# Optimization experiments

Hardware: AMD Instinct MI355X
Metric: run time of the kernel (lower is better)

Reference implementation:

```python
import jax, jax.numpy as jnp
import numpy as np

# Llama-3.2-1B-style int4-quantized decoder (4 layers, reduced vocab)
L, D, H, HD, KVH, DFF, V, B, S = 4, 2048, 32, 64, 8, 8192, 32000, 4, 1024
ROPE_THETA = 500000.0


def setup_inputs() -> dict:
    key = jax.random.key(0)
    ks = jax.random.split(key, 18)
    def qw(k, shape):  # int4 weights stored in int32 carrier, range [-8, 8)
        return jax.random.randint(k, shape, -8, 8, dtype=jnp.int32)
    def sc(k, shape):  # per-output-channel dequant scales
        return jax.random.uniform(k, shape, jnp.float32, 0.005, 0.02)
    DKV = KVH * HD
    return {
        "token_ids": jax.random.randint(ks[0], (B, S), 0, V, dtype=jnp.int32),
        "embed": jax.random.normal(ks[1], (V, D), jnp.float32) * 0.02,
        "gamma_attn": jnp.ones((L, D), jnp.float32),
        "gamma_mlp": jnp.ones((L, D), jnp.float32),
        "gamma_final": jnp.ones((D,), jnp.float32),
        "wq": qw(ks[2], (L, D, D)),   "sq": sc(ks[3], (L, D)),
        "wk": qw(ks[4], (L, DKV, D)), "sk": sc(ks[5], (L, DKV)),
        "wv": qw(ks[6], (L, DKV, D)), "sv": sc(ks[7], (L, DKV)),
        "wo": qw(ks[8], (L, D, D)),   "so": sc(ks[9], (L, D)),
        "wg": qw(ks[10], (L, DFF, D)), "sg": sc(ks[11], (L, DFF)),
        "wu": qw(ks[12], (L, DFF, D)), "su": sc(ks[13], (L, DFF)),
        "wd": qw(ks[14], (L, D, DFF)), "sd": sc(ks[15], (L, D)),
    }


def _rmsnorm(x, g, eps=1e-5):
    return x * jax.lax.rsqrt(jnp.mean(x * x, axis=-1, keepdims=True) + eps) * g


def _rope(x):  # x: [B, S, n_heads, HD], split-half rotation (Llama convention)
    half = HD // 2
    inv_freq = ROPE_THETA ** (-jnp.arange(half, dtype=jnp.float32) * 2.0 / HD)
    ang = jnp.arange(x.shape[1], dtype=jnp.float32)[:, None] * inv_freq  # [S, half]
    cos = jnp.cos(ang)[None, :, None, :]
    sin = jnp.sin(ang)[None, :, None, :]
    x1, x2 = jnp.split(x, 2, axis=-1)
    return jnp.concatenate([x1 * cos - x2 * sin, x1 * sin + x2 * cos], axis=-1)


def _qlin(x, w_int, scale):
    # int4 dequant (per-out-channel symmetric) + matmul: y = x @ (w_int*scale)^T
    w = w_int.astype(jnp.float32) * scale[:, None]
    return jnp.einsum('bsd,od->bso', x, w)


def _forward(token_ids, embed, gamma_attn, gamma_mlp, gamma_final,
             wq, sq, wk, sk, wv, sv, wo, so, wg, sg, wu, su, wd, sd):
    x = embed[token_ids]                                    # [B, S, D]
    causal = jnp.tril(jnp.ones((S, S), dtype=bool))
    for l in range(L):
        # --- attention block ---
        h = _rmsnorm(x, gamma_attn[l])
        q = _qlin(h, wq[l], sq[l]).reshape(B, S, H, HD)
        k = _qlin(h, wk[l], sk[l]).reshape(B, S, KVH, HD)
        v = _qlin(h, wv[l], sv[l]).reshape(B, S, KVH, HD)
        q, k = _rope(q), _rope(k)
        k = jnp.repeat(k, H // KVH, axis=2)                 # GQA expand
        v = jnp.repeat(v, H // KVH, axis=2)
        scores = jnp.einsum('bqhd,bkhd->bhqk', q, k) / np.float32(np.sqrt(HD))
        scores = jnp.where(causal, scores, jnp.float32(-1e9))
        p = jax.nn.softmax(scores, axis=-1)
        attn = jnp.einsum('bhqk,bkhd->bqhd', p, v).reshape(B, S, D)
        x = x + _qlin(attn, wo[l], so[l])
        # --- SwiGLU MLP block ---
        h = _rmsnorm(x, gamma_mlp[l])
        g = jax.nn.silu(_qlin(h, wg[l], sg[l]))
        u = _qlin(h, wu[l], su[l])
        x = x + _qlin(g * u, wd[l], sd[l])
    x = _rmsnorm(x, gamma_final)
    # tied-embedding LM head; next-token logits at last position (decode step)
    return x[:, -1, :] @ embed.T                             # [B, V]


def reference(token_ids, embed, gamma_attn, gamma_mlp, gamma_final,
              wq, sq, wk, sk, wv, sv, wo, so, wg, sg, wu, su, wd, sd):
    return _forward(token_ids, embed, gamma_attn, gamma_mlp, gamma_final,
                    wq, sq, wk, sk, wv, sv, wo, so, wg, sg, wu, su, wd, sd)
```

## Files before the change

kernel.cpp:

```cpp
#include <hip/hip_runtime.h>
#include <hip/hip_bf16.h>

#define D_MODEL 2048
#define NH 32
#define HDIM 64
#define KVHEADS 8
#define DKV 512
#define DFF 8192
#define SEQ 1024
#define BATCH 4
#define NTOK 4096
#define VOCAB 32000
#define NLAYER 4

typedef __attribute__((ext_vector_type(8))) _Float16 f16x8;
typedef __attribute__((ext_vector_type(4))) _Float16 f16x4;
typedef __attribute__((ext_vector_type(4))) float f32x4;

static __device__ __forceinline__ void gload16(const void* g, void* l){
    __builtin_amdgcn_global_load_lds(
        (const __attribute__((address_space(1))) unsigned int*)g,
        (__attribute__((address_space(3))) unsigned int*)l, 16, 0, 0);
}

#define MFMA(d, x, y) d = __builtin_amdgcn_mfma_f32_16x16x32_f16(x, y, d, 0, 0, 0)
#define BAR()    __builtin_amdgcn_s_barrier()
#define LGK0()   do{ asm volatile("s_waitcnt lgkmcnt(0)" ::: "memory"); \
                     __builtin_amdgcn_sched_barrier(0); }while(0)
#define PRIO(x)  __builtin_amdgcn_s_setprio(x)

__global__ __launch_bounds__(256)
void gather_kernel(const int* __restrict__ tok, const float* __restrict__ embed,
                   float* __restrict__ X)
{
    int row = blockIdx.x;
    int id = tok[row];
    const float4* s = (const float4*)(embed + (size_t)id * D_MODEL);
    float4* d = (float4*)(X + (size_t)row * D_MODEL);
    d[threadIdx.x]       = s[threadIdx.x];
    d[threadIdx.x + 256] = s[threadIdx.x + 256];
}

__global__ __launch_bounds__(256)
void wconv_kernel(const int* __restrict__ W, _Float16* __restrict__ O, int n4)
{
    int i = blockIdx.x * 256 + threadIdx.x;
    if (i >= n4) return;
    int4 w = ((const int4*)W)[i];
    f16x4 o;
    o.x = (_Float16)(float)w.x; o.y = (_Float16)(float)w.y;
    o.z = (_Float16)(float)w.z; o.w = (_Float16)(float)w.w;
    ((f16x4*)O)[i] = o;
}

__global__ __launch_bounds__(256)
void rmsnorm_kernel(const float* __restrict__ X, const float* __restrict__ gamma,
                    _Float16* __restrict__ O)
{
    int row = blockIdx.x;
    const float* x = X + (size_t)row * D_MODEL;
    _Float16* o = O + (size_t)row * D_MODEL;
    int t = threadIdx.x;
    float4 v[2];
    float ss = 0.f;
#pragma unroll
    for (int i = 0; i < 2; i++){
        v[i] = *(const float4*)&x[(t + i*256)*4];
        ss += v[i].x*v[i].x + v[i].y*v[i].y + v[i].z*v[i].z + v[i].w*v[i].w;
    }
    for (int off = 32; off; off >>= 1) ss += __shfl_xor(ss, off, 64);
    __shared__ float red[4];
    __shared__ float invs;
    int lane = t & 63, wid = t >> 6;
    if (lane == 0) red[wid] = ss;
    __syncthreads();
    if (t == 0){
        float s = red[0] + red[1] + red[2] + red[3];
        invs = 1.0f / sqrtf(s / (float)D_MODEL + 1e-5f);
    }
    __syncthreads();
    float inv = invs;
#pragma unroll
    for (int i = 0; i < 2; i++){
        float4 g = *(const float4*)&gamma[(t + i*256)*4];
        f16x4 r;
        r.x = (_Float16)(v[i].x * inv * g.x); r.y = (_Float16)(v[i].y * inv * g.y);
        r.z = (_Float16)(v[i].z * inv * g.z); r.w = (_Float16)(v[i].w * inv * g.w);
        *(f16x4*)&o[(t + i*256)*4] = r;
    }
}

__global__ __launch_bounds__(256)
void final_norm_kernel(const float* __restrict__ X, const float* __restrict__ gamma,
                       float* __restrict__ XF)
{
    int b = blockIdx.x;
    const float* x = X + ((size_t)b * SEQ + SEQ - 1) * D_MODEL;
    float* o = XF + (size_t)b * D_MODEL;
    int t = threadIdx.x;
    float4 v[2];
    float ss = 0.f;
#pragma unroll
    for (int i = 0; i < 2; i++){
        v[i] = *(const float4*)&x[(t + i*256)*4];
        ss += v[i].x*v[i].x + v[i].y*v[i].y + v[i].z*v[i].z + v[i].w*v[i].w;
    }
    for (int off = 32; off; off >>= 1) ss += __shfl_xor(ss, off, 64);
    __shared__ float red[4];
    __shared__ float invs;
    int lane = t & 63, wid = t >> 6;
    if (lane == 0) red[wid] = ss;
    __syncthreads();
    if (t == 0){
        float s = red[0] + red[1] + red[2] + red[3];
        invs = 1.0f / sqrtf(s / (float)D_MODEL + 1e-5f);
    }
    __syncthreads();
    float inv = invs;
#pragma unroll
    for (int i = 0; i < 2; i++){
        float4 g = *(const float4*)&gamma[(t + i*256)*4];
        float4 r;
        r.x = v[i].x * inv * g.x; r.y = v[i].y * inv * g.y;
        r.z = v[i].z * inv * g.z; r.w = v[i].w * inv * g.w;
        *(float4*)&o[(t + i*256)*4] = r;
    }
}

__global__ __launch_bounds__(256)
void rope_f16_kernel(_Float16* __restrict__ buf, int nh, int total)
{
    int idx = blockIdx.x * 256 + threadIdx.x;
    if (idx >= total) return;
    int d = idx & 31;
    int head = (idx >> 5) % nh;
    int row = idx / (nh * 32);
    int pos = row & (SEQ - 1);
    float inv = powf(500000.0f, -(float)d * (1.0f / 32.0f));
    float ang = (float)pos * inv;
    float s, c;
    sincosf(ang, &s, &c);
    _Float16* p = buf + (size_t)row * (nh * HDIM) + head * HDIM + d;
    float x1 = (float)p[0], x2 = (float)p[32];
    p[0]  = (_Float16)(x1 * c - x2 * s);
    p[32] = (_Float16)(x1 * s + x2 * c);
}

__global__ __launch_bounds__(512, 2)
void gemm_mlp(const _Float16* __restrict__ A, const _Float16* __restrict__ WU,
              const _Float16* __restrict__ WG,
              const float* __restrict__ su, const float* __restrict__ sg,
              _Float16* __restrict__ U, int MT, int NT, int K)
{
    __shared__ __align__(16) _Float16 AS[2][256 * 64];
    __shared__ __align__(16) _Float16 US[2][128 * 64];
    __shared__ __align__(16) _Float16 GS[3][128 * 64];

    int nwg = MT * NT;
    int flat = blockIdx.x;
    int q = nwg >> 3, r = nwg & 7;
    int xcd = flat & 7, lid = flat >> 3;
    int swz = (xcd < r ? xcd * (q + 1) : r * (q + 1) + (xcd - r) * q) + lid;
    int bm = swz % MT, bn = swz / MT;
    int m0 = bm * 256, n0 = bn * 128;

    const int t = threadIdx.x;
    const int lane = t & 63, wid = t >> 6;
    const int ln15 = lane & 15, lq = lane >> 4;
    const int wm = wid >> 1, wn = wid & 1;
    const int sw = ln15 & 7;
    const int sl0 = (lq ^ sw) * 8, sl1 = ((4 + lq) ^ sw) * 8;

    const _Float16* srcA[4]; const _Float16* srcU[2]; const _Float16* srcG[2];
#pragma unroll
    for (int rr = 0; rr < 4; rr++){
        int ch = rr * 512 + t;
        int row = ch >> 3, s = (ch & 7) ^ (row & 7);
        srcA[rr] = A + (size_t)(m0 + row) * K + s * 8;
    }
#pragma unroll
    for (int rr = 0; rr < 2; rr++){
        int ch = rr * 512 + t;
        int row = ch >> 3, s = (ch & 7) ^ (row & 7);
        srcU[rr] = WU + (size_t)(n0 + row) * K + s * 8;
        srcG[rr] = WG + (size_t)(n0 + row) * K + s * 8;
    }
#define STG_A4(tile) do{ int _b = (tile) & 1; \
    gload16(srcA[0] + (size_t)(tile)*64, &AS[_b][(wid*64)*8]); \
    gload16(srcA[1] + (size_t)(tile)*64, &AS[_b][(512 + wid*64)*8]); \
    gload16(srcA[2] + (size_t)(tile)*64, &AS[_b][(1024 + wid*64)*8]); \
    gload16(srcA[3] + (size_t)(tile)*64, &AS[_b][(1536 + wid*64)*8]); }while(0)
#define STG_U2(tile) do{ int _b = (tile) & 1; \
    gload16(srcU[0] + (size_t)(tile)*64, &US[_b][(wid*64)*8]); \
    gload16(srcU[1] + (size_t)(tile)*64, &US[_b][(512 + wid*64)*8]); }while(0)
#define STG_G3(tile) do{ int _b = (tile) % 3; \
    gload16(srcG[0] + (size_t)(tile)*64, &GS[_b][(wid*64)*8]); \
    gload16(srcG[1] + (size_t)(tile)*64, &GS[_b][(512 + wid*64)*8]); }while(0)

    f32x4 accU[4][4], accG[4][4];
#pragma unroll
    for (int i = 0; i < 4; i++)
#pragma unroll
        for (int j = 0; j < 4; j++){
            accU[i][j] = (f32x4){0.f, 0.f, 0.f, 0.f};
            accG[i][j] = (f32x4){0.f, 0.f, 0.f, 0.f};
        }

    const int KT = K >> 6;

    STG_A4(0); STG_U2(0); STG_G3(0); STG_G3(1);
    asm volatile("s_waitcnt vmcnt(2)" ::: "memory");
    BAR();

    for (int kt = 0; kt < KT; ++kt){
        int cur = kt & 1, gcur = kt % 3;
        const _Float16* Ac = AS[cur];
        const _Float16* Uc = US[cur];
        const _Float16* Gc = GS[gcur];
        bool s1 = (kt + 1 < KT), s2 = (kt + 2 < KT);

        f16x8 afk0[4], afk1[4], buk0[4], buk1[4];
#pragma unroll
        for (int mf = 0; mf < 4; mf++)
            afk0[mf] = *(const f16x8*)&Ac[(wm * 64 + mf * 16 + ln15) * 64 + sl0];
#pragma unroll
        for (int nf = 0; nf < 4; nf++)
            buk0[nf] = *(const f16x8*)&Uc[(wn * 64 + nf * 16 + ln15) * 64 + sl0];
        if (s1) STG_A4(kt + 1);
        BAR(); LGK0(); PRIO(1);
#pragma unroll
        for (int mf = 0; mf < 4; mf++)
#pragma unroll
            for (int nf = 0; nf < 4; nf++)
                MFMA(accU[mf][nf], afk0[mf], buk0[nf]);
        PRIO(0); BAR();

#pragma unroll
        for (int mf = 0; mf < 4; mf++)
            afk1[mf] = *(const f16x8*)&Ac[(wm * 64 + mf * 16 + ln15) * 64 + sl1];
#pragma unroll
        for (int nf = 0; nf < 4; nf++)
            buk1[nf] = *(const f16x8*)&Uc[(wn * 64 + nf * 16 + ln15) * 64 + sl1];
        if (s1) STG_U2(kt + 1);
        BAR(); LGK0(); PRIO(1);
#pragma unroll
        for (int mf = 0; mf < 4; mf++)
#pragma unroll
            for (int nf = 0; nf < 4; nf++)
                MFMA(accU[mf][nf], afk1[mf], buk1[nf]);
        PRIO(0); BAR();

        f16x8 bgk0[4], bgk1[4];
#pragma unroll
        for (int nf = 0; nf < 4; nf++){
            bgk0[nf] = *(const f16x8*)&Gc[(wn * 64 + nf * 16 + ln15) * 64 + sl0];
            bgk1[nf] = *(const f16x8*)&Gc[(wn * 64 + nf * 16 + ln15) * 64 + sl1];
        }
        if (s2) STG_G3(kt + 2);
        BAR(); LGK0(); PRIO(1);
#pragma unroll
        for (int mf = 0; mf < 4; mf++)
#pragma unroll
            for (int nf = 0; nf < 4; nf++)
                MFMA(accG[mf][nf], afk0[mf], bgk0[nf]);
        PRIO(0); BAR();

        PRIO(1);
#pragma unroll
        for (int mf = 0; mf < 4; mf++)
#pragma unroll
            for (int nf = 0; nf < 4; nf++)
                MFMA(accG[mf][nf], afk1[mf], bgk1[nf]);
        PRIO(0);
        if (s1){
            if (s2) asm volatile("s_waitcnt vmcnt(2)" ::: "memory");
            else    asm volatile("s_waitcnt vmcnt(0)" ::: "memory");
            BAR();
            __builtin_amdgcn_sched_barrier(0);
        }
    }
#undef STG_A4
#undef STG_U2
#undef STG_G3

#pragma unroll
    for (int mf = 0; mf < 4; mf++){
        int rowb = m0 + wm * 64 + mf * 16 + lq * 4;
#pragma unroll
        for (int nf = 0; nf < 4; nf++){
            int colg = n0 + wn * 64 + nf * 16 + ln15;
            float scu = su[colg], scg = sg[colg];
#pragma unroll
            for (int rr2 = 0; rr2 < 4; rr2++){
                float uv = accU[mf][nf][rr2] * scu;
                float gv = accG[mf][nf][rr2] * scg;
                float sig = 1.0f / (1.0f + expf(-gv));
                U[(size_t)(rowb + rr2) * DFF + colg] = (_Float16)(gv * sig * uv);
            }
        }
    }
}

template<int EPI>
__global__ __launch_bounds__(512, 2)
void gemm_small(const _Float16* __restrict__ A, const _Float16* __restrict__ W,
                const float* __restrict__ sc0, const float* __restrict__ sc1,
                const float* __restrict__ sc2,
                void* __restrict__ C0, void* __restrict__ C1, void* __restrict__ C2,
                int MT, int NT, int N, int K)
{
    __shared__ __align__(16) _Float16 AS[3][128 * 64];
    __shared__ __align__(16) _Float16 BS[3][256 * 64];

    int nwg = MT * NT;
    int flat = blockIdx.x;
    int q = nwg >> 3, r = nwg & 7;
    int xcd = flat & 7, lid = flat >> 3;
    int swz = (xcd < r ? xcd * (q + 1) : r * (q + 1) + (xcd - r) * q) + lid;
    int bm = swz % MT, bn = swz / MT;
    int m0 = bm * 128, n0 = bn * 256;

    const int t = threadIdx.x;
    const int lane = t & 63, wid = t >> 6;
    const int ln15 = lane & 15, lq = lane >> 4;
    const int wm = wid >> 2, wn = wid & 3;
    const int sw = ln15 & 7;
    const int sl0 = (lq ^ sw) * 8, sl1 = ((4 + lq) ^ sw) * 8;

    const _Float16* srcA[2]; const _Float16* srcB[4];
#pragma unroll
    for (int rr = 0; rr < 2; rr++){
        int ch = rr * 512 + t;
        int row = ch >> 3, s = (ch & 7) ^ (row & 7);
        srcA[rr] = A + (size_t)(m0 + row) * K + s * 8;
    }
#pragma unroll
    for (int rr = 0; rr < 4; rr++){
        int ch = rr * 512 + t;
        int row = ch >> 3, s = (ch & 7) ^ (row & 7);
        srcB[rr] = W + (size_t)(n0 + row) * K + s * 8;
    }
#define STG_A3(tile) do{ int _b = (tile) % 3; \
    gload16(srcA[0] + (size_t)(tile)*64, &AS[_b][(wid*64)*8]); \
    gload16(srcA[1] + (size_t)(tile)*64, &AS[_b][(512 + wid*64)*8]); }while(0)
#define STG_B3(tile) do{ int _b = (tile) % 3; \
    gload16(srcB[0] + (size_t)(tile)*64, &BS[_b][(wid*64)*8]); \
    gload16(srcB[1] + (size_t)(tile)*64, &BS[_b][(512 + wid*64)*8]); \
    gload16(srcB[2] + (size_t)(tile)*64, &BS[_b][(1024 + wid*64)*8]); \
    gload16(srcB[3] + (size_t)(tile)*64, &BS[_b][(1536 + wid*64)*8]); }while(0)

    f32x4 acc[4][4];
#pragma unroll
    for (int i = 0; i < 4; i++)
#pragma unroll
        for (int j = 0; j < 4; j++) acc[i][j] = (f32x4){0.f, 0.f, 0.f, 0.f};

    const int KT = K >> 6;

    STG_A3(0); STG_B3(0); STG_A3(1); STG_B3(1);
    asm volatile("s_waitcnt vmcnt(6)" ::: "memory");
    BAR();

    for (int kt = 0; kt < KT; ++kt){
        int cur = kt % 3;
        const _Float16* Ac = AS[cur];
        const _Float16* Bc = BS[cur];
        bool s1 = (kt + 1 < KT), s2 = (kt + 2 < KT);

        f16x8 afk0[4], afk1[4], bk0[4], bk1[4];
#pragma unroll
        for (int mf = 0; mf < 4; mf++)
            afk0[mf] = *(const f16x8*)&Ac[(wm * 64 + mf * 16 + ln15) * 64 + sl0];
#pragma unroll
        for (int nf = 0; nf < 4; nf++)
            bk0[nf] = *(const f16x8*)&Bc[(wn * 64 + nf * 16 + ln15) * 64 + sl0];
        if (s2) STG_B3(kt + 2);
        BAR(); LGK0(); PRIO(1);
#pragma unroll
        for (int mf = 0; mf < 4; mf++)
#pragma unroll
            for (int nf = 0; nf < 4; nf++)
                MFMA(acc[mf][nf], afk0[mf], bk0[nf]);
        PRIO(0); BAR();

#pragma unroll
        for (int mf = 0; mf < 4; mf++)
            afk1[mf] = *(const f16x8*)&Ac[(wm * 64 + mf * 16 + ln15) * 64 + sl1];
#pragma unroll
        for (int nf = 0; nf < 4; nf++)
            bk1[nf] = *(const f16x8*)&Bc[(wn * 64 + nf * 16 + ln15) * 64 + sl1];
        if (s2) STG_A3(kt + 2);
        BAR(); LGK0(); PRIO(1);
#pragma unroll
        for (int mf = 0; mf < 4; mf++)
#pragma unroll
            for (int nf = 0; nf < 4; nf++)
                MFMA(acc[mf][nf], afk1[mf], bk1[nf]);
        PRIO(0);
        if (s1){
            if (s2) asm volatile("s_waitcnt vmcnt(6)" ::: "memory");
            else    asm volatile("s_waitcnt vmcnt(0)" ::: "memory");
            BAR();
            __builtin_amdgcn_sched_barrier(0);
        }
    }
#undef STG_A3
#undef STG_B3

    if (EPI == 3){
        const float* sp; _Float16* dp; int nloc, nstr;
        if (n0 < 2048)      { sp = sc0; dp = (_Float16*)C0; nloc = n0;        nstr = 2048; }
        else if (n0 < 2560) { sp = sc1; dp = (_Float16*)C1; nloc = n0 - 2048; nstr = 512; }
        else                { sp = sc2; dp = (_Float16*)C2; nloc = n0 - 2560; nstr = 512; }
#pragma unroll
        for (int mf = 0; mf < 4; mf++){
            int rowb = m0 + wm * 64 + mf * 16 + lq * 4;
#pragma unroll
            for (int nf = 0; nf < 4; nf++){
                int colg = wn * 64 + nf * 16 + ln15;
                float sc = sp[nloc + colg];
#pragma unroll
                for (int rr2 = 0; rr2 < 4; rr2++)
                    dp[(size_t)(rowb + rr2) * nstr + nloc + colg] =
                        (_Float16)(acc[mf][nf][rr2] * sc);
            }
        }
    } else {
#pragma unroll
        for (int mf = 0; mf < 4; mf++){
            int rowb = m0 + wm * 64 + mf * 16 + lq * 4;
#pragma unroll
            for (int nf = 0; nf < 4; nf++){
                int colg = n0 + wn * 64 + nf * 16 + ln15;
                float sc = sc0[colg];
#pragma unroll
                for (int rr2 = 0; rr2 < 4; rr2++){
                    size_t idx = (size_t)(rowb + rr2) * N + colg;
                    float val = acc[mf][nf][rr2] * sc;
                    if (EPI == 0){
                        ((_Float16*)C0)[idx] = (_Float16)val;
                    } else {
                        ((float*)C0)[idx] += val;
                    }
                }
            }
        }
    }
}

__global__ __launch_bounds__(256)
void attn_kernel(const _Float16* __restrict__ Qb, const _Float16* __restrict__ Kb,
                 const _Float16* __restrict__ Vb, _Float16* __restrict__ Ob)
{
    int bid = blockIdx.x;
    int qt = bid & 7, h = (bid >> 3) & 31, b = bid >> 8;
    int kvh = h >> 2;
    int q0 = qt * 128;
    int t = threadIdx.x, lane = t & 63, wid = t >> 6;
    int ln15 = lane & 15, lq = lane >> 4;

    __shared__ __align__(16) _Float16 Ksm[64 * 72];
    __shared__ __align__(16) _Float16 Vt[64 * 72];
    __shared__ __align__(16) _Float16 Pl[128 * 72];

    f16x8 qf[2][2];
    int qrow_g = b * SEQ + q0 + wid * 32;
#pragma unroll
    for (int mf = 0; mf < 2; mf++)
#pragma unroll
        for (int dc = 0; dc < 2; dc++)
            qf[mf][dc] = *(const f16x8*)(Qb + (size_t)(qrow_g + mf * 16 + ln15) * D_MODEL
                                         + h * HDIM + dc * 32 + lq * 8);

    f32x4 outv[2][4];
#pragma unroll
    for (int i = 0; i < 2; i++)
#pragma unroll
        for (int j = 0; j < 4; j++) outv[i][j] = (f32x4){0.f, 0.f, 0.f, 0.f};
    float mrun[2][4], lrun[2][4];
#pragma unroll
    for (int i = 0; i < 2; i++)
#pragma unroll
        for (int r = 0; r < 4; r++){ mrun[i][r] = -1e30f; lrun[i][r] = 0.f; }

    int ntile = (q0 + 128) >> 6;
    for (int kt = 0; kt < ntile; kt++){
        f16x8 k8[2], v8[2];
#pragma unroll
        for (int i = 0; i < 2; i++){
            int f = t + i * 256;
            int row = f >> 3, c8 = f & 7;
            size_t base = (size_t)(b * SEQ + kt * 64 + row) * DKV + kvh * HDIM + c8 * 8;
            k8[i] = *(const f16x8*)&Kb[base];
            v8[i] = *(const f16x8*)&Vb[base];
        }
        __syncthreads();
#pragma unroll
        for (int i = 0; i < 2; i++){
            int f = t + i * 256;
            int row = f >> 3, c8 = f & 7;
            *(f16x8*)&Ksm[row * 72 + c8 * 8] = k8[i];
#pragma unroll
            for (int j = 0; j < 8; j++)
                Vt[(c8 * 8 + j) * 72 + row] = v8[i][j];
        }
        __syncthreads();

#pragma unroll
        for (int mf = 0; mf < 2; mf++){
            f32x4 sa[4];
#pragma unroll
            for (int kvf = 0; kvf < 4; kvf++) sa[kvf] = (f32x4){0.f, 0.f, 0.f, 0.f};
#pragma unroll
            for (int kvf = 0; kvf < 4; kvf++)
#pragma unroll
                for (int dc = 0; dc < 2; dc++){
                    f16x8 kb = *(const f16x8*)&Ksm[(kvf * 16 + ln15) * 72 + dc * 32 + lq * 8];
                    sa[kvf] = __builtin_amdgcn_mfma_f32_16x16x32_f16(qf[mf][dc], kb, sa[kvf], 0, 0, 0);
                }
            int qbase = q0 + wid * 32 + mf * 16 + lq * 4;
            float rowmax[4] = {-1e30f, -1e30f, -1e30f, -1e30f};
#pragma unroll
            for (int kvf = 0; kvf < 4; kvf++){
                int kva = kt * 64 + kvf * 16 + ln15;
#pragma unroll
                for (int r = 0; r < 4; r++){
                    float sv = sa[kvf][r] * 0.125f;
                    if (kva > qbase + r) sv = -1e9f;
                    sa[kvf][r] = sv;
                    rowmax[r] = fmaxf(rowmax[r], sv);
                }
            }
#pragma unroll
            for (int r = 0; r < 4; r++){
                rowmax[r] = fmaxf(rowmax[r], __shfl_xor(rowmax[r], 1, 64));
                rowmax[r] = fmaxf(rowmax[r], __shfl_xor(rowmax[r], 2, 64));
                rowmax[r] = fmaxf(rowmax[r], __shfl_xor(rowmax[r], 4, 64));
                rowmax[r] = fmaxf(rowmax[r], __shfl_xor(rowmax[r], 8, 64));
            }
            float scl[4], rsum[4];
#pragma unroll
            for (int r = 0; r < 4; r++){
                float mo = mrun[mf][r];
                float mn = fmaxf(mo, rowmax[r]);
                scl[r] = expf(mo - mn);
                mrun[mf][r] = mn;
                rsum[r] = 0.f;
            }
#pragma unroll
            for (int kvf = 0; kvf < 4; kvf++)
#pragma unroll
                for (int r = 0; r < 4; r++){
                    float p = expf(sa[kvf][r] - mrun[mf][r]);
                    sa[kvf][r] = p;
                    rsum[r] += p;
                }
#pragma unroll
            for (int r = 0; r < 4; r++){
                rsum[r] += __shfl_xor(rsum[r], 1, 64);
                rsum[r] += __shfl_xor(rsum[r], 2, 64);
                rsum[r] += __shfl_xor(rsum[r], 4, 64);
                rsum[r] += __shfl_xor(rsum[r], 8, 64);
                lrun[mf][r] = lrun[mf][r] * scl[r] + rsum[r];
            }
#pragma unroll
            for (int dfr = 0; dfr < 4; dfr++)
#pragma unroll
                for (int r = 0; r < 4; r++) outv[mf][dfr][r] *= scl[r];
#pragma unroll
            for (int kvf = 0; kvf < 4; kvf++)
#pragma unroll
                for (int r = 0; r < 4; r++)
                    Pl[(wid * 32 + mf * 16 + lq * 4 + r) * 72 + kvf * 16 + ln15] = (_Float16)sa[kvf][r];
        }
        __syncthreads();

#pragma unroll
        for (int mf = 0; mf < 2; mf++)
#pragma unroll
            for (int kc = 0; kc < 2; kc++){
                f16x8 pa = *(const f16x8*)&Pl[(wid * 32 + mf * 16 + ln15) * 72 + kc * 32 + lq * 8];
#pragma unroll
                for (int dfr = 0; dfr < 4; dfr++){
                    f16x8 vb = *(const f16x8*)&Vt[(dfr * 16 + ln15) * 72 + kc * 32 + lq * 8];
                    outv[mf][dfr] = __builtin_amdgcn_mfma_f32_16x16x32_f16(pa, vb, outv[mf][dfr], 0, 0, 0);
                }
            }
    }

#pragma unroll
    for (int mf = 0; mf < 2; mf++)
#pragma unroll
        for (int dfr = 0; dfr < 4; dfr++)
#pragma unroll
            for (int r = 0; r < 4; r++){
                float val = outv[mf][dfr][r] / lrun[mf][r];
                size_t row = (size_t)(b * SEQ + q0 + wid * 32 + mf * 16 + lq * 4 + r);
                Ob[row * D_MODEL + h * HDIM + dfr * 16 + ln15] = (_Float16)val;
            }
}

__global__ __launch_bounds__(256)
void lmhead_kernel(const float* __restrict__ XF, const float* __restrict__ embed,
                   float* __restrict__ out)
{
    __shared__ float xl[4 * D_MODEL];
    int t = threadIdx.x;
#pragma unroll
    for (int i = 0; i < 8; i++){
        int f = t + i * 256;
        ((float4*)xl)[f] = ((const float4*)XF)[f];
    }
    __syncthreads();
    int lane = t & 63, wid = t >> 6;
    for (int rr = 0; rr < 16; rr++){
        int vrow = blockIdx.x * 64 + wid * 16 + rr;
        const float4* er = (const float4*)(embed + (size_t)vrow * D_MODEL);
        float acc[4] = {0.f, 0.f, 0.f, 0.f};
        for (int j = 0; j < 8; j++){
            float4 e = er[lane + 64 * j];
#pragma unroll
            for (int b = 0; b < 4; b++){
                float4 xv = ((float4*)xl)[b * 512 + lane + 64 * j];
                acc[b] += e.x * xv.x + e.y * xv.y + e.z * xv.z + e.w * xv.w;
            }
        }
#pragma unroll
        for (int b = 0; b < 4; b++)
            for (int off = 32; off; off >>= 1) acc[b] += __shfl_xor(acc[b], off, 64);
        if (lane == 0){
#pragma unroll
            for (int b = 0; b < 4; b++)
                out[(size_t)b * VOCAB + vrow] = acc[b];
        }
    }
}

extern "C" void kernel_launch(void* const* d_in, const int* in_sizes, int n_in,
                              void* d_out, int out_size, void* d_ws, size_t ws_size,
                              hipStream_t stream)
{
    const int*   tok   = (const int*)d_in[0];
    const float* embed = (const float*)d_in[1];
    const float* g_attn = (const float*)d_in[2];
    const float* g_mlp  = (const float*)d_in[3];
    const float* g_fin  = (const float*)d_in[4];
    const int*   wq = (const int*)d_in[5];  const float* sq = (const float*)d_in[6];
    const int*   wk = (const int*)d_in[7];  const float* sk = (const float*)d_in[8];
    const int*   wv = (const int*)d_in[9];  const float* sv = (const float*)d_in[10];
    const int*   wo = (const int*)d_in[11]; const float* so = (const float*)d_in[12];
    const int*   wg = (const int*)d_in[13]; const float* sg = (const float*)d_in[14];
    const int*   wu = (const int*)d_in[15]; const float* su = (const float*)d_in[16];
    const int*   wd = (const int*)d_in[17]; const float* sd = (const float*)d_in[18];
    float* out = (float*)d_out;

    char* p = (char*)d_ws;
    _Float16* Wf = (_Float16*)p;  p += (size_t)60817408 * 2;
    float*    X  = (float*)p;     p += (size_t)NTOK * D_MODEL * 4;
    _Float16* Hb = (_Float16*)p;  p += (size_t)NTOK * D_MODEL * 2;
    _Float16* Qb = (_Float16*)p;  p += (size_t)NTOK * D_MODEL * 2;
    _Float16* Kb = (_Float16*)p;  p += (size_t)NTOK * DKV * 2;
    _Float16* Vb = (_Float16*)p;  p += (size_t)NTOK * DKV * 2;
    _Float16* Ab = (_Float16*)p;  p += (size_t)NTOK * D_MODEL * 2;
    _Float16* Ub = (_Float16*)p;  p += (size_t)NTOK * DFF * 2;
    float*    XF = (float*)p;     p += (size_t)BATCH * D_MODEL * 4;

    _Float16* wqf = Wf;
    _Float16* wkf = wqf + (size_t)D_MODEL * D_MODEL;
    _Float16* wvf = wkf + (size_t)DKV * D_MODEL;
    _Float16* wof = wvf + (size_t)DKV * D_MODEL;
    _Float16* wgf = wof + (size_t)D_MODEL * D_MODEL;
    _Float16* wuf = wgf + (size_t)DFF * D_MODEL;
    _Float16* wdf = wuf + (size_t)DFF * D_MODEL;

    gather_kernel<<<NTOK, 256, 0, stream>>>(tok, embed, X);

    for (int l = 0; l < NLAYER; l++){
        {
            const int nDD = D_MODEL * D_MODEL / 4, nKD = DKV * D_MODEL / 4, nFD = DFF * D_MODEL / 4;
            wconv_kernel<<<(nDD + 255) / 256, 256, 0, stream>>>(wq + (size_t)l * D_MODEL * D_MODEL, wqf, nDD);
            wconv_kernel<<<(nKD + 255) / 256, 256, 0, stream>>>(wk + (size_t)l * DKV * D_MODEL, wkf, nKD);
            wconv_kernel<<<(nKD + 255) / 256, 256, 0, stream>>>(wv + (size_t)l * DKV * D_MODEL, wvf, nKD);
            wconv_kernel<<<(nDD + 255) / 256, 256, 0, stream>>>(wo + (size_t)l * D_MODEL * D_MODEL, wof, nDD);
            wconv_kernel<<<(nFD + 255) / 256, 256, 0, stream>>>(wg + (size_t)l * DFF * D_MODEL, wgf, nFD);
            wconv_kernel<<<(nFD + 255) / 256, 256, 0, stream>>>(wu + (size_t)l * DFF * D_MODEL, wuf, nFD);
            wconv_kernel<<<(nFD + 255) / 256, 256, 0, stream>>>(wd + (size_t)l * D_MODEL * DFF, wdf, nFD);
        }

        rmsnorm_kernel<<<NTOK, 256, 0, stream>>>(X, g_attn + (size_t)l * D_MODEL, Hb);
        gemm_small<3><<<32 * 12, 512, 0, stream>>>(Hb, wqf,
            sq + (size_t)l * D_MODEL, sk + (size_t)l * DKV, sv + (size_t)l * DKV,
            Qb, Kb, Vb, 32, 12, 3072, D_MODEL);
        {
            int totq = NTOK * NH * 32;
            rope_f16_kernel<<<(totq + 255) / 256, 256, 0, stream>>>(Qb, NH, totq);
            int totk = NTOK * KVHEADS * 32;
            rope_f16_kernel<<<(totk + 255) / 256, 256, 0, stream>>>(Kb, KVHEADS, totk);
        }
        attn_kernel<<<1024, 256, 0, stream>>>(Qb, Kb, Vb, Ab);
        gemm_small<1><<<32 * 8, 512, 0, stream>>>(Ab, wof,
            so + (size_t)l * D_MODEL, nullptr, nullptr,
            X, nullptr, nullptr, 32, 8, D_MODEL, D_MODEL);

        rmsnorm_kernel<<<NTOK, 256, 0, stream>>>(X, g_mlp + (size_t)l * D_MODEL, Hb);
        gemm_mlp<<<16 * 64, 512, 0, stream>>>(Hb, wuf, wgf,
            su + (size_t)l * DFF, sg + (size_t)l * DFF, Ub, 16, 64, D_MODEL);
        gemm_small<1><<<32 * 8, 512, 0, stream>>>(Ub, wdf,
            sd + (size_t)l * D_MODEL, nullptr, nullptr,
            X, nullptr, nullptr, 32, 8, D_MODEL, DFF);
    }

    final_norm_kernel<<<BATCH, 256, 0, stream>>>(X, g_fin, XF);
    lmhead_kernel<<<VOCAB / 64, 256, 0, stream>>>(XF, embed, out);
}
```

Baseline: 3.625 ms.

## Collapse GEMM main loops to one barrier per k-tile with prefetch at top

In both the fused gate/up SwiGLU GEMM and the generic GEMM, the per-k-tile schedule drops its four (or two) barrier and lgkmcnt phases and the s_setprio toggles. Each iteration now does one vmcnt wait and one barrier at the top, issues all global-to-LDS prefetches for later tiles at once, then runs the LDS fragment reads and MFMAs with no further sync. The aim is to cut barrier stalls and let the compiler interleave ds_reads with MFMAs. In exchange it gives up explicit control over how waves interleave and over MFMA priority, and the compiler schedule may raise register pressure.

```diff
diff --git a/kernel.cpp b/kernel.cpp
--- a/kernel.cpp
+++ b/kernel.cpp
@@ -25,9 +25,6 @@
 
 #define MFMA(d, x, y) d = __builtin_amdgcn_mfma_f32_16x16x32_f16(x, y, d, 0, 0, 0)
 #define BAR()    __builtin_amdgcn_s_barrier()
-#define LGK0()   do{ asm volatile("s_waitcnt lgkmcnt(0)" ::: "memory"); \
-                     __builtin_amdgcn_sched_barrier(0); }while(0)
-#define PRIO(x)  __builtin_amdgcn_s_setprio(x)
 
 __global__ __launch_bounds__(256)
 void gather_kernel(const int* __restrict__ tok, const float* __restrict__ embed,
@@ -209,8 +206,6 @@
     const int KT = K >> 6;
 
     STG_A4(0); STG_U2(0); STG_G3(0); STG_G3(1);
-    asm volatile("s_waitcnt vmcnt(2)" ::: "memory");
-    BAR();
 
     for (int kt = 0; kt < KT; ++kt){
         int cur = kt & 1, gcur = kt % 3;
@@ -219,65 +214,53 @@
         const _Float16* Gc = GS[gcur];
         bool s1 = (kt + 1 < KT), s2 = (kt + 2 < KT);
 
-        f16x8 afk0[4], afk1[4], buk0[4], buk1[4];
-#pragma unroll
-        for (int mf = 0; mf < 4; mf++)
-            afk0[mf] = *(const f16x8*)&Ac[(wm * 64 + mf * 16 + ln15) * 64 + sl0];
+        if (s1) asm volatile("s_waitcnt vmcnt(2)" ::: "memory");
+        else    asm volatile("s_waitcnt vmcnt(0)" ::: "memory");
+        BAR();
+        __builtin_amdgcn_sched_barrier(0);
+
+        if (s1){ STG_A4(kt + 1); STG_U2(kt + 1); }
+        if (s2){ STG_G3(kt + 2); }
+
+        f16x8 af0[4], af1[4], bu0[4], bu1[4], bg0[4], bg1[4];
+#pragma unroll
+        for (int mf = 0; mf < 4; mf++)
+            af0[mf] = *(const f16x8*)&Ac[(wm * 64 + mf * 16 + ln15) * 64 + sl0];
 #pragma unroll
         for (int nf = 0; nf < 4; nf++)
-            buk0[nf] = *(const f16x8*)&Uc[(wn * 64 + nf * 16 + ln15) * 64 + sl0];
-        if (s1) STG_A4(kt + 1);
-        BAR(); LGK0(); PRIO(1);
+            bu0[nf] = *(const f16x8*)&Uc[(wn * 64 + nf * 16 + ln15) * 64 + sl0];
 #pragma unroll
         for (int mf = 0; mf < 4; mf++)
 #pragma unroll
             for (int nf = 0; nf < 4; nf++)
-                MFMA(accU[mf][nf], afk0[mf], buk0[nf]);
-        PRIO(0); BAR();
-
-#pragma unroll
-        for (int mf = 0; mf < 4; mf++)
-            afk1[mf] = *(const f16x8*)&Ac[(wm * 64 + mf * 16 + ln15) * 64 + sl1];
+                MFMA(accU[mf][nf], af0[mf], bu0[nf]);
 #pragma unroll
         for (int nf = 0; nf < 4; nf++)
-            buk1[nf] = *(const f16x8*)&Uc[(wn * 64 + nf * 16 + ln15) * 64 + sl1];
-        if (s1) STG_U2(kt + 1);
-        BAR(); LGK0(); PRIO(1);
+            bg0[nf] = *(const f16x8*)&Gc[(wn * 64 + nf * 16 + ln15) * 64 + sl0];
 #pragma unroll
         for (int mf = 0; mf < 4; mf++)
 #pragma unroll
             for (int nf = 0; nf < 4; nf++)
-                MFMA(accU[mf][nf], afk1[mf], buk1[nf]);
-        PRIO(0); BAR();
-
-        f16x8 bgk0[4], bgk1[4];
-#pragma unroll
-        for (int nf = 0; nf < 4; nf++){
-            bgk0[nf] = *(const f16x8*)&Gc[(wn * 64 + nf * 16 + ln15) * 64 + sl0];
-            bgk1[nf] = *(const f16x8*)&Gc[(wn * 64 + nf * 16 + ln15) * 64 + sl1];
-        }
-        if (s2) STG_G3(kt + 2);
-        BAR(); LGK0(); PRIO(1);
+                MFMA(accG[mf][nf], af0[mf], bg0[nf]);
+#pragma unroll
+        for (int mf = 0; mf < 4; mf++)
+            af1[mf] = *(const f16x8*)&Ac[(wm * 64 + mf * 16 + ln15) * 64 + sl1];
+#pragma unroll
+        for (int nf = 0; nf < 4; nf++)
+            bu1[nf] = *(const f16x8*)&Uc[(wn * 64 + nf * 16 + ln15) * 64 + sl1];
 #pragma unroll
         for (int mf = 0; mf < 4; mf++)
 #pragma unroll
             for (int nf = 0; nf < 4; nf++)
-                MFMA(accG[mf][nf], afk0[mf], bgk0[nf]);
-        PRIO(0); BAR();
-
-        PRIO(1);
+                MFMA(accU[mf][nf], af1[mf], bu1[nf]);
+#pragma unroll
+        for (int nf = 0; nf < 4; nf++)
+            bg1[nf] = *(const f16x8*)&Gc[(wn * 64 + nf * 16 + ln15) * 64 + sl1];
 #pragma unroll
         for (int mf = 0; mf < 4; mf++)
 #pragma unroll
             for (int nf = 0; nf < 4; nf++)
-                MFMA(accG[mf][nf], afk1[mf], bgk1[nf]);
-        PRIO(0);
-        if (s1){
-            if (s2) asm volatile("s_waitcnt vmcnt(2)" ::: "memory");
-            else    asm volatile("s_waitcnt vmcnt(0)" ::: "memory");
-            BAR();
-            __builtin_amdgcn_sched_barrier(0);
-        }
+                MFMA(accG[mf][nf], af1[mf], bg1[nf]);
     }
 #undef STG_A4
 #undef STG_U2
@@ -358,8 +341,6 @@
     const int KT = K >> 6;
 
     STG_A3(0); STG_B3(0); STG_A3(1); STG_B3(1);
-    asm volatile("s_waitcnt vmcnt(6)" ::: "memory");
-    BAR();
 
     for (int kt = 0; kt < KT; ++kt){
         int cur = kt % 3;
@@ -367,42 +348,36 @@
         const _Float16* Bc = BS[cur];
         bool s1 = (kt + 1 < KT), s2 = (kt + 2 < KT);
 
-        f16x8 afk0[4], afk1[4], bk0[4], bk1[4];
-#pragma unroll
-        for (int mf = 0; mf < 4; mf++)
-            afk0[mf] = *(const f16x8*)&Ac[(wm * 64 + mf * 16 + ln15) * 64 + sl0];
+        if (s1) asm volatile("s_waitcnt vmcnt(6)" ::: "memory");
+        else    asm volatile("s_waitcnt vmcnt(0)" ::: "memory");
+        BAR();
+        __builtin_amdgcn_sched_barrier(0);
+
+        if (s2){ STG_B3(kt + 2); STG_A3(kt + 2); }
+
+        f16x8 af0[4], af1[4], bk0[4], bk1[4];
+#pragma unroll
+        for (int mf = 0; mf < 4; mf++)
+            af0[mf] = *(const f16x8*)&Ac[(wm * 64 + mf * 16 + ln15) * 64 + sl0];
 #pragma unroll
         for (int nf = 0; nf < 4; nf++)
             bk0[nf] = *(const f16x8*)&Bc[(wn * 64 + nf * 16 + ln15) * 64 + sl0];
-        if (s2) STG_B3(kt + 2);
-        BAR(); LGK0(); PRIO(1);
 #pragma unroll
         for (int mf = 0; mf < 4; mf++)
 #pragma unroll
             for (int nf = 0; nf < 4; nf++)
-                MFMA(acc[mf][nf], afk0[mf], bk0[nf]);
-        PRIO(0); BAR();
-
-#pragma unroll
-        for (int mf = 0; mf < 4; mf++)
-            afk1[mf] = *(const f16x8*)&Ac[(wm * 64 + mf * 16 + ln15) * 64 + sl1];
+                MFMA(acc[mf][nf], af0[mf], bk0[nf]);
+#pragma unroll
+        for (int mf = 0; mf < 4; mf++)
+            af1[mf] = *(const f16x8*)&Ac[(wm * 64 + mf * 16 + ln15) * 64 + sl1];
 #pragma unroll
         for (int nf = 0; nf < 4; nf++)
             bk1[nf] = *(const f16x8*)&Bc[(wn * 64 + nf * 16 + ln15) * 64 + sl1];
-        if (s2) STG_A3(kt + 2);
-        BAR(); LGK0(); PRIO(1);
 #pragma unroll
         for (int mf = 0; mf < 4; mf++)
 #pragma unroll
             for (int nf = 0; nf < 4; nf++)
-                MFMA(acc[mf][nf], afk1[mf], bk1[nf]);
-        PRIO(0);
-        if (s1){
-            if (s2) asm volatile("s_waitcnt vmcnt(6)" ::: "memory");
-            else    asm volatile("s_waitcnt vmcnt(0)" ::: "memory");
-            BAR();
-            __builtin_amdgcn_sched_barrier(0);
-        }
+                MFMA(acc[mf][nf], af1[mf], bk1[nf]);
     }
 #undef STG_A3
 #undef STG_B3
```

Result: slower. 4.098 ms (+13.1%).

## Fuse RoPE into QKV GEMM epilogue and prefetch K/V tiles in attention

Applied to the files above, without the earlier changes.

Replaces the separate RoPE kernels with a precomputed cos/sin table and applies the rotation in the QKV GEMM epilogue. Each wave's 64-column span covers one head, so elements d and d+32 sit in registers nf and nf+2. The attention kernel now register-prefetches the next K/V tile while computing on the current one. This removes two extra read/write passes over Q and K per layer and hides global load latency in attention, at the cost of more registers and table lookups in the epilogue.

```diff
diff --git a/kernel.cpp b/kernel.cpp
--- a/kernel.cpp
+++ b/kernel.cpp
@@ -42,6 +42,18 @@
 }
 
 __global__ __launch_bounds__(256)
+void rope_table_kernel(float2* __restrict__ rt)
+{
+    int idx = blockIdx.x * 256 + threadIdx.x;
+    int pos = idx >> 5, d = idx & 31;
+    float inv = powf(500000.0f, -(float)d * (1.0f / 32.0f));
+    float ang = (float)pos * inv;
+    float s, c;
+    sincosf(ang, &s, &c);
+    rt[idx] = make_float2(c, s);
+}
+
+__global__ __launch_bounds__(256)
 void wconv_kernel(const int* __restrict__ W, _Float16* __restrict__ O, int n4)
 {
     int i = blockIdx.x * 256 + threadIdx.x;
@@ -125,25 +137,6 @@
         r.z = v[i].z * inv * g.z; r.w = v[i].w * inv * g.w;
         *(float4*)&o[(t + i*256)*4] = r;
     }
-}
-
-__global__ __launch_bounds__(256)
-void rope_f16_kernel(_Float16* __restrict__ buf, int nh, int total)
-{
-    int idx = blockIdx.x * 256 + threadIdx.x;
-    if (idx >= total) return;
-    int d = idx & 31;
-    int head = (idx >> 5) % nh;
-    int row = idx / (nh * 32);
-    int pos = row & (SEQ - 1);
-    float inv = powf(500000.0f, -(float)d * (1.0f / 32.0f));
-    float ang = (float)pos * inv;
-    float s, c;
-    sincosf(ang, &s, &c);
-    _Float16* p = buf + (size_t)row * (nh * HDIM) + head * HDIM + d;
-    float x1 = (float)p[0], x2 = (float)p[32];
-    p[0]  = (_Float16)(x1 * c - x2 * s);
-    p[32] = (_Float16)(x1 * s + x2 * c);
 }
 
 __global__ __launch_bounds__(512, 2)
@@ -307,6 +300,7 @@
                 const float* __restrict__ sc0, const float* __restrict__ sc1,
                 const float* __restrict__ sc2,
                 void* __restrict__ C0, void* __restrict__ C1, void* __restrict__ C2,
+                const float2* __restrict__ rt,
                 int MT, int NT, int N, int K)
 {
     __shared__ __align__(16) _Float16 AS[3][128 * 64];
@@ -367,10 +361,10 @@
         const _Float16* Bc = BS[cur];
         bool s1 = (kt + 1 < KT), s2 = (kt + 2 < KT);
 
-        f16x8 afk0[4], afk1[4], bk0[4], bk1[4];
-#pragma unroll
-        for (int mf = 0; mf < 4; mf++)
-            afk0[mf] = *(const f16x8*)&Ac[(wm * 64 + mf * 16 + ln15) * 64 + sl0];
+        f16x8 af0[4], af1[4], bk0[4], bk1[4];
+#pragma unroll
+        for (int mf = 0; mf < 4; mf++)
+            af0[mf] = *(const f16x8*)&Ac[(wm * 64 + mf * 16 + ln15) * 64 + sl0];
 #pragma unroll
         for (int nf = 0; nf < 4; nf++)
             bk0[nf] = *(const f16x8*)&Bc[(wn * 64 + nf * 16 + ln15) * 64 + sl0];
@@ -380,12 +374,12 @@
         for (int mf = 0; mf < 4; mf++)
 #pragma unroll
             for (int nf = 0; nf < 4; nf++)
-                MFMA(acc[mf][nf], afk0[mf], bk0[nf]);
+                MFMA(acc[mf][nf], af0[mf], bk0[nf]);
         PRIO(0); BAR();
 
 #pragma unroll
         for (int mf = 0; mf < 4; mf++)
-            afk1[mf] = *(const f16x8*)&Ac[(wm * 64 + mf * 16 + ln15) * 64 + sl1];
+            af1[mf] = *(const f16x8*)&Ac[(wm * 64 + mf * 16 + ln15) * 64 + sl1];
 #pragma unroll
         for (int nf = 0; nf < 4; nf++)
             bk1[nf] = *(const f16x8*)&Bc[(wn * 64 + nf * 16 + ln15) * 64 + sl1];
@@ -395,7 +389,7 @@
         for (int mf = 0; mf < 4; mf++)
 #pragma unroll
             for (int nf = 0; nf < 4; nf++)
-                MFMA(acc[mf][nf], afk1[mf], bk1[nf]);
+                MFMA(acc[mf][nf], af1[mf], bk1[nf]);
         PRIO(0);
         if (s1){
             if (s2) asm volatile("s_waitcnt vmcnt(6)" ::: "memory");
@@ -412,17 +406,41 @@
         if (n0 < 2048)      { sp = sc0; dp = (_Float16*)C0; nloc = n0;        nstr = 2048; }
         else if (n0 < 2560) { sp = sc1; dp = (_Float16*)C1; nloc = n0 - 2048; nstr = 512; }
         else                { sp = sc2; dp = (_Float16*)C2; nloc = n0 - 2560; nstr = 512; }
-#pragma unroll
-        for (int mf = 0; mf < 4; mf++){
-            int rowb = m0 + wm * 64 + mf * 16 + lq * 4;
-#pragma unroll
-            for (int nf = 0; nf < 4; nf++){
-                int colg = wn * 64 + nf * 16 + ln15;
-                float sc = sp[nloc + colg];
-#pragma unroll
-                for (int rr2 = 0; rr2 < 4; rr2++)
-                    dp[(size_t)(rowb + rr2) * nstr + nloc + colg] =
-                        (_Float16)(acc[mf][nf][rr2] * sc);
+        bool dorope = (n0 < 2560);
+        if (dorope){
+#pragma unroll
+            for (int mf = 0; mf < 4; mf++){
+                int rowb = m0 + wm * 64 + mf * 16 + lq * 4;
+#pragma unroll
+                for (int nf = 0; nf < 2; nf++){
+                    int colg = wn * 64 + nf * 16 + ln15;
+                    int d = nf * 16 + ln15;
+                    float s1v = sp[nloc + colg], s2v = sp[nloc + colg + 32];
+#pragma unroll
+                    for (int rr2 = 0; rr2 < 4; rr2++){
+                        int row = rowb + rr2;
+                        int pos = row & (SEQ - 1);
+                        float2 cs = rt[pos * 32 + d];
+                        float x1 = acc[mf][nf][rr2] * s1v;
+                        float x2 = acc[mf][nf + 2][rr2] * s2v;
+                        dp[(size_t)row * nstr + nloc + colg]      = (_Float16)(x1 * cs.x - x2 * cs.y);
+                        dp[(size_t)row * nstr + nloc + colg + 32] = (_Float16)(x1 * cs.y + x2 * cs.x);
+                    }
+                }
+            }
+        } else {
+#pragma unroll
+            for (int mf = 0; mf < 4; mf++){
+                int rowb = m0 + wm * 64 + mf * 16 + lq * 4;
+#pragma unroll
+                for (int nf = 0; nf < 4; nf++){
+                    int colg = wn * 64 + nf * 16 + ln15;
+                    float sc = sp[nloc + colg];
+#pragma unroll
+                    for (int rr2 = 0; rr2 < 4; rr2++)
+                        dp[(size_t)(rowb + rr2) * nstr + nloc + colg] =
+                            (_Float16)(acc[mf][nf][rr2] * sc);
+                }
             }
         }
     } else {
@@ -484,27 +502,35 @@
         for (int r = 0; r < 4; r++){ mrun[i][r] = -1e30f; lrun[i][r] = 0.f; }
 
     int ntile = (q0 + 128) >> 6;
+    int ld_row = (t + 0) >> 3, ld_c8 = t & 7;
+    int ld_row1 = (t + 256) >> 3;
+
+    f16x8 k8[2], v8[2];
+    {
+        size_t base0 = (size_t)(b * SEQ + ld_row) * DKV + kvh * HDIM + ld_c8 * 8;
+        size_t base1 = (size_t)(b * SEQ + ld_row1) * DKV + kvh * HDIM + ld_c8 * 8;
+        k8[0] = *(const f16x8*)&Kb[base0];  v8[0] = *(const f16x8*)&Vb[base0];
+        k8[1] = *(const f16x8*)&Kb[base1];  v8[1] = *(const f16x8*)&Vb[base1];
+    }
+
     for (int kt = 0; kt < ntile; kt++){
-        f16x8 k8[2], v8[2];
+        __syncthreads();
 #pragma unroll
         for (int i = 0; i < 2; i++){
-            int f = t + i * 256;
-            int row = f >> 3, c8 = f & 7;
-            size_t base = (size_t)(b * SEQ + kt * 64 + row) * DKV + kvh * HDIM + c8 * 8;
-            k8[i] = *(const f16x8*)&Kb[base];
-            v8[i] = *(const f16x8*)&Vb[base];
+            int row = (i == 0) ? ld_row : ld_row1;
+            *(f16x8*)&Ksm[row * 72 + ld_c8 * 8] = k8[i];
+#pragma unroll
+            for (int j = 0; j < 8; j++)
+                Vt[(ld_c8 * 8 + j) * 72 + row] = v8[i][j];
         }
         __syncthreads();
-#pragma unroll
-        for (int i = 0; i < 2; i++){
-            int f = t + i * 256;
-            int row = f >> 3, c8 = f & 7;
-            *(f16x8*)&Ksm[row * 72 + c8 * 8] = k8[i];
-#pragma unroll
-            for (int j = 0; j < 8; j++)
-                Vt[(c8 * 8 + j) * 72 + row] = v8[i][j];
-        }
-        __syncthreads();
+
+        if (kt + 1 < ntile){
+            size_t base0 = (size_t)(b * SEQ + (kt + 1) * 64 + ld_row) * DKV + kvh * HDIM + ld_c8 * 8;
+            size_t base1 = (size_t)(b * SEQ + (kt + 1) * 64 + ld_row1) * DKV + kvh * HDIM + ld_c8 * 8;
+            k8[0] = *(const f16x8*)&Kb[base0];  v8[0] = *(const f16x8*)&Vb[base0];
+            k8[1] = *(const f16x8*)&Kb[base1];  v8[1] = *(const f16x8*)&Vb[base1];
+        }
 
 #pragma unroll
         for (int mf = 0; mf < 2; mf++){
@@ -664,6 +690,7 @@
     _Float16* Ab = (_Float16*)p;  p += (size_t)NTOK * D_MODEL * 2;
     _Float16* Ub = (_Float16*)p;  p += (size_t)NTOK * DFF * 2;
     float*    XF = (float*)p;     p += (size_t)BATCH * D_MODEL * 4;
+    float2*   RT = (float2*)p;    p += (size_t)SEQ * 32 * 8;
 
     _Float16* wqf = Wf;
     _Float16* wkf = wqf + (size_t)D_MODEL * D_MODEL;
@@ -674,6 +701,7 @@
     _Float16* wdf = wuf + (size_t)DFF * D_MODEL;
 
     gather_kernel<<<NTOK, 256, 0, stream>>>(tok, embed, X);
+    rope_table_kernel<<<SEQ * 32 / 256, 256, 0, stream>>>(RT);
 
     for (int l = 0; l < NLAYER; l++){
         {
@@ -690,24 +718,18 @@
         rmsnorm_kernel<<<NTOK, 256, 0, stream>>>(X, g_attn + (size_t)l * D_MODEL, Hb);
         gemm_small<3><<<32 * 12, 512, 0, stream>>>(Hb, wqf,
             sq + (size_t)l * D_MODEL, sk + (size_t)l * DKV, sv + (size_t)l * DKV,
-            Qb, Kb, Vb, 32, 12, 3072, D_MODEL);
-        {
-            int totq = NTOK * NH * 32;
-            rope_f16_kernel<<<(totq + 255) / 256, 256, 0, stream>>>(Qb, NH, totq);
-            int totk = NTOK * KVHEADS * 32;
-            rope_f16_kernel<<<(totk + 255) / 256, 256, 0, stream>>>(Kb, KVHEADS, totk);
-        }
+            Qb, Kb, Vb, RT, 32, 12, 3072, D_MODEL);
         attn_kernel<<<1024, 256, 0, stream>>>(Qb, Kb, Vb, Ab);
         gemm_small<1><<<32 * 8, 512, 0, stream>>>(Ab, wof,
             so + (size_t)l * D_MODEL, nullptr, nullptr,
-            X, nullptr, nullptr, 32, 8, D_MODEL, D_MODEL);
+            X, nullptr, nullptr, nullptr, 32, 8, D_MODEL, D_MODEL);
 
         rmsnorm_kernel<<<NTOK, 256, 0, stream>>>(X, g_mlp + (size_t)l * D_MODEL, Hb);
         gemm_mlp<<<16 * 64, 512, 0, stream>>>(Hb, wuf, wgf,
             su + (size_t)l * DFF, sg + (size_t)l * DFF, Ub, 16, 64, D_MODEL);
         gemm_small<1><<<32 * 8, 512, 0, stream>>>(Ub, wdf,
             sd + (size_t)l * D_MODEL, nullptr, nullptr,
-            X, nullptr, nullptr, 32, 8, D_MODEL, DFF);
+            X, nullptr, nullptr, nullptr, 32, 8, D_MODEL, DFF);
     }
 
     final_norm_kernel<<<BATCH, 256, 0, stream>>>(X, g_fin, XF);
```

Result: faster. 3.520 ms (-2.9%).
